# Kernel tuning notes

Measured on AMD Instinct MI355X. Metric: run time of the kernel, lower is better.

The kernel has to match this reference:

```python
import jax, jax.numpy as jnp
import numpy as np

N_NODES = 50000
N_EDGES = 800000
IN_C, HID_C, OUT_C = 128, 128, 64


def setup_inputs() -> dict:
    key = jax.random.key(0)
    k = jax.random.split(key, 8)
    x = jax.random.normal(k[0], (N_NODES, IN_C), dtype=jnp.float32)
    edge_index = jax.random.randint(k[1], (2, N_EDGES), 0, N_NODES, dtype=jnp.int64)
    edge_weight = jax.random.uniform(k[2], (N_EDGES,), dtype=jnp.float32)
    # GCNConv parameters (glorot-style scale)
    W1 = jax.random.normal(k[3], (IN_C, HID_C), dtype=jnp.float32) * (1.0 / np.sqrt(IN_C))
    b1 = jnp.zeros((HID_C,), dtype=jnp.float32)
    W2 = jax.random.normal(k[4], (HID_C, OUT_C), dtype=jnp.float32) * (1.0 / np.sqrt(HID_C))
    b2 = jnp.zeros((OUT_C,), dtype=jnp.float32)
    return {"x": x, "edge_index": edge_index, "edge_weight": edge_weight,
            "W1": W1, "b1": b1, "W2": W2, "b2": b2}


def _gcn_conv(x, src, dst, edge_weight, W, b, num_nodes):
    # GCNConv(normalize=False): out[i] = sum_{(j->i) in E} w_ji * (x[j] @ W) + b
    h = x @ W                                  # [N, C_out] dense GEMM first (cheaper than per-edge)
    msg = h[src]                               # [E, C_out] gather
    if edge_weight is not None:
        msg = msg * edge_weight[:, None]
    agg = jax.ops.segment_sum(msg, dst, num_segments=num_nodes)  # scatter-add
    return agg + b


def reference(x, edge_index, edge_weight, W1, b1, W2, b2):
    # Eval mode: F.dropout(training=False) is identity.
    src, dst = edge_index[0], edge_index[1]
    n = x.shape[0]
    h = _gcn_conv(x, src, dst, edge_weight, W1, b1, n)
    h = jax.nn.relu(h)
    out = _gcn_conv(h, src, dst, None, W2, b2, n)  # second conv: no edge_weight
    return out
```

## Files before the change

kernel.cpp:

```cpp
#include <hip/hip_runtime.h>
#include <hip/hip_fp8.h>

#define N_NODES 50000
#define N_EDGES 800000
#define IN_C    128
#define HID_C   128
#define OUT_C   64

#define EPB     4096
#define SC_BLOCKS 196
#define NBUCKET 196
#define CAP     6144
#define G1_BLOCKS 782

typedef unsigned int       uint32;
typedef unsigned short     ushort16;
typedef unsigned char      uchar8;
typedef unsigned long long u64;
typedef __attribute__((ext_vector_type(8))) short short8;
typedef __attribute__((ext_vector_type(4))) float f32x4;

__device__ __forceinline__ ushort16 f2bf(float f) {
    uint32 u = __float_as_uint(f);
    u += 0x7FFFu + ((u >> 16) & 1u);
    return (ushort16)(u >> 16);
}
__device__ __forceinline__ ushort16 f2h_bits(float f) {
    union { _Float16 h; ushort16 u; } cv;
    cv.h = (_Float16)f;
    return cv.u;
}
__device__ __forceinline__ float h_bits2f(uint32 bits) {
    union { ushort16 u; _Float16 h; } cv;
    cv.u = (ushort16)bits;
    return (float)cv.h;
}
__device__ __forceinline__ uchar8 f2fp8(float f) {
    __hip_fp8_e4m3 t(f);
    return *reinterpret_cast<unsigned char*>(&t);
}
__device__ __forceinline__ float fp82f(uchar8 b) {
    __hip_fp8_e4m3 t;
    *reinterpret_cast<unsigned char*>(&t) = b;
    return (float)t;
}
__device__ __forceinline__ void fp8x4_wacc(uint32 v, float w, f32x4& a) {
    a.x += w * fp82f((uchar8)(v & 0xFF));
    a.y += w * fp82f((uchar8)((v >> 8) & 0xFF));
    a.z += w * fp82f((uchar8)((v >> 16) & 0xFF));
    a.w += w * fp82f((uchar8)(v >> 24));
}
__device__ __forceinline__ void fp8x4_acc(uint32 v, f32x4& a) {
    a.x += fp82f((uchar8)(v & 0xFF));
    a.y += fp82f((uchar8)((v >> 8) & 0xFF));
    a.z += fp82f((uchar8)((v >> 16) & 0xFF));
    a.w += fp82f((uchar8)(v >> 24));
}
__device__ __forceinline__ void bfly4(f32x4& a, int d) {
    a.x += __shfl_xor(a.x, d); a.y += __shfl_xor(a.y, d);
    a.z += __shfl_xor(a.z, d); a.w += __shfl_xor(a.w, d);
}
__device__ __forceinline__ uint32 packbf(float a, float b) {
    return (uint32)f2bf(a) | ((uint32)f2bf(b) << 16);
}

__global__ __launch_bounds__(256) void prep_w_kernel(const float* __restrict__ W1,
                                                     const float* __restrict__ W2,
                                                     ushort16* __restrict__ W1t,
                                                     ushort16* __restrict__ W2t,
                                                     int* __restrict__ cursorC) {
    if (blockIdx.x == 0 && threadIdx.x < NBUCKET) cursorC[threadIdx.x] = 0;
    int i = blockIdx.x * 256 + threadIdx.x;
    if (i < 128 * 128) {
        int n = i / 128, k = i % 128;
        W1t[i] = f2bf(W1[k * 128 + n]);
    }
    int j = i - 128 * 128;
    if (j >= 0 && j < 64 * 128) {
        int n = j / 128, k = j % 128;
        W2t[j] = f2bf(W2[k * 64 + n]);
    }
}

__global__ __launch_bounds__(256) void gemm1_scatter_kernel(const float* __restrict__ x,
                                                            const ushort16* __restrict__ W1t,
                                                            uchar8* __restrict__ H1,
                                                            const int* __restrict__ ei,
                                                            const float* __restrict__ ew,
                                                            int* __restrict__ cursorC,
                                                            u64* __restrict__ ebuf) {
    __shared__ char smem[52224];
    const int tid = threadIdx.x;

    if (blockIdx.x < SC_BLOCKS) {
        int* hist  = (int*)smem;
        int* lbase = (int*)(smem + 1024);
        int blk = blockIdx.x;
        hist[tid] = 0;
        __syncthreads();
        int base = blk * EPB;
        int    bv[EPB / 256];
        uint32 pkv[EPB / 256];
        ushort16 wv[EPB / 256];
#pragma unroll
        for (int k = 0; k < EPB / 256; k++) {
            int e = base + tid + k * 256;
            if (e < N_EDGES) {
                int dst = ei[N_EDGES + e];
                int src = ei[e];
                float w = ew[e];
                bv[k]  = dst >> 8;
                pkv[k] = ((uint32)(dst & 255) << 16) | (uint32)src;
                wv[k]  = f2h_bits(w);
                atomicAdd(&hist[bv[k]], 1);
            } else bv[k] = -1;
        }
        __syncthreads();
        int n = hist[tid];
        lbase[tid] = n ? atomicAdd(&cursorC[tid], n) : 0;
        __syncthreads();
        hist[tid] = 0;
        __syncthreads();
#pragma unroll
        for (int k = 0; k < EPB / 256; k++) {
            if (bv[k] >= 0) {
                int b = bv[k];
                int r = atomicAdd(&hist[b], 1);
                int pos = lbase[b] + r;
                if (pos < CAP)
                    ebuf[(size_t)b * CAP + pos] = ((u64)wv[k] << 32) | pkv[k];
            }
        }
        return;
    }

    typedef ushort16 row136[136];
    row136* As = (row136*)smem;
    row136* Ws = (row136*)(smem + 64 * 136 * 2);

    const int wave = tid >> 6;
    const int lane = tid & 63;
    const int quad = lane >> 4;
    const int m    = lane & 15;
    const int blockRow = (blockIdx.x - SC_BLOCKS) * 64;

#pragma unroll
    for (int p = 0; p < 8; p++) {
        int u = tid + 256 * p;
        int row = u / 16, c8 = u % 16;
        uint4 v = ((const uint4*)W1t)[u];
        *((uint4*)&Ws[row][c8 * 8]) = v;
    }
#pragma unroll
    for (int p = 0; p < 8; p++) {
        int u = tid + 256 * p;
        int row = u / 32, c4 = u % 32;
        int gr = blockRow + row; if (gr > N_NODES - 1) gr = N_NODES - 1;
        float4 v = ((const float4*)x)[gr * 32 + c4];
        ushort4 s;
        s.x = f2bf(v.x); s.y = f2bf(v.y); s.z = f2bf(v.z); s.w = f2bf(v.w);
        *((ushort4*)&As[row][c4 * 4]) = s;
    }
    __syncthreads();

    f32x4 acc[8];
#pragma unroll
    for (int nt = 0; nt < 8; nt++) acc[nt] = (f32x4){0.f, 0.f, 0.f, 0.f};

#pragma unroll
    for (int kc = 0; kc < 128; kc += 32) {
        short8 a = *((const short8*)&As[wave * 16 + m][kc + quad * 8]);
#pragma unroll
        for (int nt = 0; nt < 8; nt++) {
            short8 b = *((const short8*)&Ws[nt * 16 + m][kc + quad * 8]);
            acc[nt] = __builtin_amdgcn_mfma_f32_16x16x32_bf16(a, b, acc[nt], 0, 0, 0);
        }
    }

    __syncthreads();
    uchar8* c8lds = (uchar8*)&As[0][0];
#pragma unroll
    for (int nt = 0; nt < 8; nt++)
#pragma unroll
        for (int r = 0; r < 4; r++)
            c8lds[(wave * 16 + quad * 4 + r) * 128 + nt * 16 + m] = f2fp8(acc[nt][r]);
    __syncthreads();
#pragma unroll
    for (int p = 0; p < 2; p++) {
        int u = tid + 256 * p;
        int row = u / 8, c16 = u % 8;
        int gr = blockRow + row;
        if (gr < N_NODES)
            ((uint4*)H1)[gr * 8 + c16] = *((const uint4*)&c8lds[row * 128 + c16 * 16]);
    }
}

__global__ __launch_bounds__(1024) void csr_fine_kernel(const u64* __restrict__ ebuf,
                                                        const int* __restrict__ cursorC,
                                                        int* __restrict__ rowStart,
                                                        int* __restrict__ rowEnd,
                                                        uint32* __restrict__ pairs) {
    __shared__ uint32   keys[CAP];
    __shared__ ushort16 ws[CAP];
    __shared__ int hist[256];
    __shared__ int scan[256];
    int b = blockIdx.x, t = threadIdx.x;
    int s = b * CAP;
    int len = cursorC[b];
    if (len > CAP) len = CAP;
    if (t < 256) hist[t] = 0;
    __syncthreads();
    for (int j = t; j < len; j += 1024) {
        u64 kv = ebuf[s + j];
        uint32 lo = (uint32)kv;
        keys[j] = lo;
        ws[j]   = (ushort16)(kv >> 32);
        atomicAdd(&hist[lo >> 16], 1);
    }
    __syncthreads();
    if (t < 256) scan[t] = hist[t];
    __syncthreads();
    for (int off = 1; off < 256; off <<= 1) {
        int a = 0;
        if (t < 256 && t >= off) a = scan[t - off];
        __syncthreads();
        if (t < 256) scan[t] += a;
        __syncthreads();
    }
    if (t < 256) {
        int excl = scan[t] - hist[t];
        hist[t] = excl;
        int node = b * 256 + t;
        if (node < N_NODES) {
            rowStart[node] = s + excl;
            rowEnd[node]   = s + scan[t];
        }
    }
    __syncthreads();
    for (int j = t; j < len; j += 1024) {
        uint32 kv = keys[j];
        int r = atomicAdd(&hist[kv >> 16], 1);
        pairs[s + r] = (kv & 0xFFFFu) | ((uint32)ws[j] << 16);
    }
}

template<int NT, bool ABF16, bool OUTFP8>
__global__ __launch_bounds__(256) void mfma_gemm_kernel(const void* __restrict__ Aptr,
                                                        const ushort16* __restrict__ Wt,
                                                        void* __restrict__ Cout, int M) {
    constexpr int N = NT * 16;
    __shared__ ushort16 As[64][136];
    __shared__ ushort16 Ws[N][136];

    const int tid  = threadIdx.x;
    const int wave = tid >> 6;
    const int lane = tid & 63;
    const int quad = lane >> 4;
    const int m    = lane & 15;
    const int blockRow = blockIdx.x * 64;

#pragma unroll
    for (int p = 0; p < N * 16 / 256; p++) {
        int u = tid + 256 * p;
        int row = u / 16, c8 = u % 16;
        uint4 v = ((const uint4*)Wt)[u];
        *((uint4*)&Ws[row][c8 * 8]) = v;
    }
    if (ABF16) {
#pragma unroll
        for (int p = 0; p < 4; p++) {
            int u = tid + 256 * p;
            int row = u / 16, c8 = u % 16;
            int gr = blockRow + row; if (gr > M - 1) gr = M - 1;
            uint4 v = ((const uint4*)Aptr)[gr * 16 + c8];
            *((uint4*)&As[row][c8 * 8]) = v;
        }
    } else {
#pragma unroll
        for (int p = 0; p < 8; p++) {
            int u = tid + 256 * p;
            int row = u / 32, c4 = u % 32;
            int gr = blockRow + row; if (gr > M - 1) gr = M - 1;
            float4 v = ((const float4*)Aptr)[gr * 32 + c4];
            ushort4 s;
            s.x = f2bf(v.x); s.y = f2bf(v.y); s.z = f2bf(v.z); s.w = f2bf(v.w);
            *((ushort4*)&As[row][c4 * 4]) = s;
        }
    }
    __syncthreads();

    f32x4 acc[NT];
#pragma unroll
    for (int nt = 0; nt < NT; nt++) acc[nt] = (f32x4){0.f, 0.f, 0.f, 0.f};

#pragma unroll
    for (int kc = 0; kc < 128; kc += 32) {
        short8 a = *((const short8*)&As[wave * 16 + m][kc + quad * 8]);
#pragma unroll
        for (int nt = 0; nt < NT; nt++) {
            short8 b = *((const short8*)&Ws[nt * 16 + m][kc + quad * 8]);
            acc[nt] = __builtin_amdgcn_mfma_f32_16x16x32_bf16(a, b, acc[nt], 0, 0, 0);
        }
    }

    __syncthreads();
    if (OUTFP8) {
        uchar8* c8lds = (uchar8*)&As[0][0];
#pragma unroll
        for (int nt = 0; nt < NT; nt++)
#pragma unroll
            for (int r = 0; r < 4; r++)
                c8lds[(wave * 16 + quad * 4 + r) * N + nt * 16 + m] = f2fp8(acc[nt][r]);
        __syncthreads();
#pragma unroll
        for (int p = 0; p < 64 * N / 16 / 256; p++) {
            int u = tid + 256 * p;
            int row = u / (N / 16), c16 = u % (N / 16);
            int gr = blockRow + row;
            if (gr < M)
                ((uint4*)Cout)[gr * (N / 16) + c16] = *((const uint4*)&c8lds[row * N + c16 * 16]);
        }
    } else {
#pragma unroll
        for (int nt = 0; nt < NT; nt++)
#pragma unroll
            for (int r = 0; r < 4; r++)
                As[wave * 16 + quad * 4 + r][nt * 16 + m] = f2bf(acc[nt][r]);
        __syncthreads();
#pragma unroll
        for (int p = 0; p < 64 * N / 8 / 256; p++) {
            int u = tid + 256 * p;
            int row = u / (N / 8), c8 = u % (N / 8);
            int gr = blockRow + row;
            if (gr < M)
                ((uint4*)Cout)[gr * (N / 8) + c8] = *((const uint4*)&As[row][c8 * 8]);
        }
    }
}

__global__ __launch_bounds__(256) void agg1_kernel(const uint4* __restrict__ H1,
                                                   const int* __restrict__ rowStart,
                                                   const int* __restrict__ rowEnd,
                                                   const uint32* __restrict__ pairs,
                                                   const float* __restrict__ b1,
                                                   uint4* __restrict__ A1) {
    int node = blockIdx.x * 4 + (threadIdx.x >> 6);
    int lane = threadIdx.x & 63;
    int oct = lane >> 3, cl = lane & 7;
    if (node >= N_NODES) return;
    int s = rowStart[node], e = rowEnd[node];
    f32x4 aA = (f32x4){0.f,0.f,0.f,0.f}, aB = aA, aC = aA, aD = aA;
    int i = s + oct;
    for (; i + 8 < e; i += 16) {
        uint32 p0 = pairs[i], p1 = pairs[i + 8];
        uint4 h0 = H1[(p0 & 0xFFFFu) * 8 + cl];
        uint4 h1 = H1[(p1 & 0xFFFFu) * 8 + cl];
        float w0 = h_bits2f(p0 >> 16), w1 = h_bits2f(p1 >> 16);
        fp8x4_wacc(h0.x, w0, aA); fp8x4_wacc(h0.y, w0, aB);
        fp8x4_wacc(h0.z, w0, aC); fp8x4_wacc(h0.w, w0, aD);
        fp8x4_wacc(h1.x, w1, aA); fp8x4_wacc(h1.y, w1, aB);
        fp8x4_wacc(h1.z, w1, aC); fp8x4_wacc(h1.w, w1, aD);
    }
    for (; i < e; i += 8) {
        uint32 p = pairs[i];
        uint4 h = H1[(p & 0xFFFFu) * 8 + cl];
        float w = h_bits2f(p >> 16);
        fp8x4_wacc(h.x, w, aA); fp8x4_wacc(h.y, w, aB);
        fp8x4_wacc(h.z, w, aC); fp8x4_wacc(h.w, w, aD);
    }
#pragma unroll
    for (int d = 8; d <= 32; d <<= 1) {
        bfly4(aA, d); bfly4(aB, d); bfly4(aC, d); bfly4(aD, d);
    }
    if (oct == 0) {
        const float4* b1f = (const float4*)b1;
        float4 b0 = b1f[cl * 4], b4 = b1f[cl * 4 + 1], b8 = b1f[cl * 4 + 2], bc = b1f[cl * 4 + 3];
        uint4 r0, r1;
        r0.x = packbf(fmaxf(aA.x + b0.x, 0.f), fmaxf(aA.y + b0.y, 0.f));
        r0.y = packbf(fmaxf(aA.z + b0.z, 0.f), fmaxf(aA.w + b0.w, 0.f));
        r0.z = packbf(fmaxf(aB.x + b4.x, 0.f), fmaxf(aB.y + b4.y, 0.f));
        r0.w = packbf(fmaxf(aB.z + b4.z, 0.f), fmaxf(aB.w + b4.w, 0.f));
        r1.x = packbf(fmaxf(aC.x + b8.x, 0.f), fmaxf(aC.y + b8.y, 0.f));
        r1.y = packbf(fmaxf(aC.z + b8.z, 0.f), fmaxf(aC.w + b8.w, 0.f));
        r1.z = packbf(fmaxf(aD.x + bc.x, 0.f), fmaxf(aD.y + bc.y, 0.f));
        r1.w = packbf(fmaxf(aD.z + bc.z, 0.f), fmaxf(aD.w + bc.w, 0.f));
        A1[node * 16 + cl * 2]     = r0;
        A1[node * 16 + cl * 2 + 1] = r1;
    }
}

__global__ __launch_bounds__(256) void agg2_kernel(const uint2* __restrict__ H2,
                                                   const int* __restrict__ rowStart,
                                                   const int* __restrict__ rowEnd,
                                                   const uint32* __restrict__ pairs,
                                                   const float* __restrict__ b2,
                                                   float4* __restrict__ out) {
    int node = blockIdx.x * 4 + (threadIdx.x >> 6);
    int lane = threadIdx.x & 63;
    int oct = lane >> 3, cl = lane & 7;
    if (node >= N_NODES) return;
    int s = rowStart[node], e = rowEnd[node];
    f32x4 aX = (f32x4){0.f,0.f,0.f,0.f}, aY = aX;
    int i = s + oct;
    for (; i + 8 < e; i += 16) {
        uint32 p0 = pairs[i], p1 = pairs[i + 8];
        uint2 v0 = H2[(p0 & 0xFFFFu) * 8 + cl];
        uint2 v1 = H2[(p1 & 0xFFFFu) * 8 + cl];
        fp8x4_acc(v0.x, aX); fp8x4_acc(v0.y, aY);
        fp8x4_acc(v1.x, aX); fp8x4_acc(v1.y, aY);
    }
    for (; i < e; i += 8) {
        uint2 v = H2[(pairs[i] & 0xFFFFu) * 8 + cl];
        fp8x4_acc(v.x, aX); fp8x4_acc(v.y, aY);
    }
#pragma unroll
    for (int d = 8; d <= 32; d <<= 1) { bfly4(aX, d); bfly4(aY, d); }
    if (oct == 0) {
        const float4* b2f = (const float4*)b2;
        float4 bx = b2f[cl * 2], by = b2f[cl * 2 + 1];
        float4 rx, ry;
        rx.x = aX.x + bx.x; rx.y = aX.y + bx.y; rx.z = aX.z + bx.z; rx.w = aX.w + bx.w;
        ry.x = aY.x + by.x; ry.y = aY.y + by.y; ry.z = aY.z + by.z; ry.w = aY.w + by.w;
        out[node * 16 + cl * 2]     = rx;
        out[node * 16 + cl * 2 + 1] = ry;
    }
}

extern "C" void kernel_launch(void* const* d_in, const int* in_sizes, int n_in,
                              void* d_out, int out_size, void* d_ws, size_t ws_size,
                              hipStream_t stream) {
    const float* x  = (const float*)d_in[0];
    const int*   ei = (const int*)  d_in[1];
    const float* ew = (const float*)d_in[2];
    const float* W1 = (const float*)d_in[3];
    const float* b1 = (const float*)d_in[4];
    const float* W2 = (const float*)d_in[5];
    const float* b2 = (const float*)d_in[6];
    float* out = (float*)d_out;

    uint32* H1      = (uint32*)d_ws;
    uint32* A1      = H1 + (size_t)N_NODES * 32;
    uint32* H2      = A1 + (size_t)N_NODES * 64;
    uint32* pairs   = H2 + (size_t)N_NODES * 16;
    u64* ebuf       = (u64*)(pairs + (size_t)NBUCKET * CAP);
    ushort16* W1t   = (ushort16*)(ebuf + (size_t)NBUCKET * CAP);
    ushort16* W2t   = W1t + 128 * 128;
    int* cursorC    = (int*)(W2t + 64 * 128);
    int* rowStart   = cursorC + ((NBUCKET + 1) & ~1);
    int* rowEnd     = rowStart + N_NODES;

    const int nodeBlocks = (N_NODES + 3) / 4;

    prep_w_kernel<<<96, 256, 0, stream>>>(W1, W2, W1t, W2t, cursorC);

    gemm1_scatter_kernel<<<SC_BLOCKS + G1_BLOCKS, 256, 0, stream>>>(
        x, W1t, (uchar8*)H1, ei, ew, cursorC, ebuf);

    csr_fine_kernel<<<NBUCKET, 1024, 0, stream>>>(ebuf, cursorC, rowStart, rowEnd, pairs);

    agg1_kernel<<<nodeBlocks, 256, 0, stream>>>((const uint4*)H1, rowStart, rowEnd, pairs, b1, (uint4*)A1);

    mfma_gemm_kernel<4, true, true><<<G1_BLOCKS, 256, 0, stream>>>(A1, W2t, H2, N_NODES);

    agg2_kernel<<<nodeBlocks, 256, 0, stream>>>((const uint2*)H2, rowStart, rowEnd, pairs, b2, (float4*)out);
}
```

Measured before the change: 164.2 us.

## Drop weight-prep kernel, convert weights inline, and double scatter block count

```diff
diff --git a/kernel.cpp b/kernel.cpp
--- a/kernel.cpp
+++ b/kernel.cpp
@@ -7,8 +7,8 @@
 #define HID_C   128
 #define OUT_C   64
 
-#define EPB     4096
-#define SC_BLOCKS 196
+#define EPB     2048
+#define SC_BLOCKS 391
 #define NBUCKET 196
 #define CAP     6144
 #define G1_BLOCKS 782
@@ -64,26 +64,8 @@
     return (uint32)f2bf(a) | ((uint32)f2bf(b) << 16);
 }
 
-__global__ __launch_bounds__(256) void prep_w_kernel(const float* __restrict__ W1,
-                                                     const float* __restrict__ W2,
-                                                     ushort16* __restrict__ W1t,
-                                                     ushort16* __restrict__ W2t,
-                                                     int* __restrict__ cursorC) {
-    if (blockIdx.x == 0 && threadIdx.x < NBUCKET) cursorC[threadIdx.x] = 0;
-    int i = blockIdx.x * 256 + threadIdx.x;
-    if (i < 128 * 128) {
-        int n = i / 128, k = i % 128;
-        W1t[i] = f2bf(W1[k * 128 + n]);
-    }
-    int j = i - 128 * 128;
-    if (j >= 0 && j < 64 * 128) {
-        int n = j / 128, k = j % 128;
-        W2t[j] = f2bf(W2[k * 64 + n]);
-    }
-}
-
 __global__ __launch_bounds__(256) void gemm1_scatter_kernel(const float* __restrict__ x,
-                                                            const ushort16* __restrict__ W1t,
+                                                            const float* __restrict__ W1,
                                                             uchar8* __restrict__ H1,
                                                             const int* __restrict__ ei,
                                                             const float* __restrict__ ew,
@@ -147,9 +129,11 @@
 #pragma unroll
     for (int p = 0; p < 8; p++) {
         int u = tid + 256 * p;
-        int row = u / 16, c8 = u % 16;
-        uint4 v = ((const uint4*)W1t)[u];
-        *((uint4*)&Ws[row][c8 * 8]) = v;
+        int n = u & 127, k0 = (u >> 7) * 8;
+        ushort16 tmp[8];
+#pragma unroll
+        for (int j = 0; j < 8; j++) tmp[j] = f2bf(W1[(k0 + j) * 128 + n]);
+        *((uint4*)&Ws[n][k0]) = *((const uint4*)tmp);
     }
 #pragma unroll
     for (int p = 0; p < 8; p++) {
@@ -244,13 +228,11 @@
     }
 }
 
-template<int NT, bool ABF16, bool OUTFP8>
-__global__ __launch_bounds__(256) void mfma_gemm_kernel(const void* __restrict__ Aptr,
-                                                        const ushort16* __restrict__ Wt,
-                                                        void* __restrict__ Cout, int M) {
-    constexpr int N = NT * 16;
+__global__ __launch_bounds__(256) void gemm2_kernel(const uint32* __restrict__ A1,
+                                                    const float* __restrict__ W2,
+                                                    uchar8* __restrict__ H2) {
     __shared__ ushort16 As[64][136];
-    __shared__ ushort16 Ws[N][136];
+    __shared__ ushort16 Ws[64][136];
 
     const int tid  = threadIdx.x;
     const int wave = tid >> 6;
@@ -260,81 +242,52 @@
     const int blockRow = blockIdx.x * 64;
 
 #pragma unroll
-    for (int p = 0; p < N * 16 / 256; p++) {
+    for (int p = 0; p < 4; p++) {
+        int u = tid + 256 * p;
+        int n = u & 63, k0 = (u >> 6) * 8;
+        ushort16 tmp[8];
+#pragma unroll
+        for (int j = 0; j < 8; j++) tmp[j] = f2bf(W2[(k0 + j) * 64 + n]);
+        *((uint4*)&Ws[n][k0]) = *((const uint4*)tmp);
+    }
+#pragma unroll
+    for (int p = 0; p < 4; p++) {
         int u = tid + 256 * p;
         int row = u / 16, c8 = u % 16;
-        uint4 v = ((const uint4*)Wt)[u];
-        *((uint4*)&Ws[row][c8 * 8]) = v;
-    }
-    if (ABF16) {
-#pragma unroll
-        for (int p = 0; p < 4; p++) {
-            int u = tid + 256 * p;
-            int row = u / 16, c8 = u % 16;
-            int gr = blockRow + row; if (gr > M - 1) gr = M - 1;
-            uint4 v = ((const uint4*)Aptr)[gr * 16 + c8];
-            *((uint4*)&As[row][c8 * 8]) = v;
-        }
-    } else {
-#pragma unroll
-        for (int p = 0; p < 8; p++) {
-            int u = tid + 256 * p;
-            int row = u / 32, c4 = u % 32;
-            int gr = blockRow + row; if (gr > M - 1) gr = M - 1;
-            float4 v = ((const float4*)Aptr)[gr * 32 + c4];
-            ushort4 s;
-            s.x = f2bf(v.x); s.y = f2bf(v.y); s.z = f2bf(v.z); s.w = f2bf(v.w);
-            *((ushort4*)&As[row][c4 * 4]) = s;
-        }
-    }
-    __syncthreads();
-
-    f32x4 acc[NT];
-#pragma unroll
-    for (int nt = 0; nt < NT; nt++) acc[nt] = (f32x4){0.f, 0.f, 0.f, 0.f};
+        int gr = blockRow + row; if (gr > N_NODES - 1) gr = N_NODES - 1;
+        uint4 v = ((const uint4*)A1)[gr * 16 + c8];
+        *((uint4*)&As[row][c8 * 8]) = v;
+    }
+    __syncthreads();
+
+    f32x4 acc[4];
+#pragma unroll
+    for (int nt = 0; nt < 4; nt++) acc[nt] = (f32x4){0.f, 0.f, 0.f, 0.f};
 
 #pragma unroll
     for (int kc = 0; kc < 128; kc += 32) {
         short8 a = *((const short8*)&As[wave * 16 + m][kc + quad * 8]);
 #pragma unroll
-        for (int nt = 0; nt < NT; nt++) {
+        for (int nt = 0; nt < 4; nt++) {
             short8 b = *((const short8*)&Ws[nt * 16 + m][kc + quad * 8]);
             acc[nt] = __builtin_amdgcn_mfma_f32_16x16x32_bf16(a, b, acc[nt], 0, 0, 0);
         }
     }
 
     __syncthreads();
-    if (OUTFP8) {
-        uchar8* c8lds = (uchar8*)&As[0][0];
-#pragma unroll
-        for (int nt = 0; nt < NT; nt++)
-#pragma unroll
-            for (int r = 0; r < 4; r++)
-                c8lds[(wave * 16 + quad * 4 + r) * N + nt * 16 + m] = f2fp8(acc[nt][r]);
-        __syncthreads();
-#pragma unroll
-        for (int p = 0; p < 64 * N / 16 / 256; p++) {
-            int u = tid + 256 * p;
-            int row = u / (N / 16), c16 = u % (N / 16);
-            int gr = blockRow + row;
-            if (gr < M)
-                ((uint4*)Cout)[gr * (N / 16) + c16] = *((const uint4*)&c8lds[row * N + c16 * 16]);
-        }
-    } else {
-#pragma unroll
-        for (int nt = 0; nt < NT; nt++)
-#pragma unroll
-            for (int r = 0; r < 4; r++)
-                As[wave * 16 + quad * 4 + r][nt * 16 + m] = f2bf(acc[nt][r]);
-        __syncthreads();
-#pragma unroll
-        for (int p = 0; p < 64 * N / 8 / 256; p++) {
-            int u = tid + 256 * p;
-            int row = u / (N / 8), c8 = u % (N / 8);
-            int gr = blockRow + row;
-            if (gr < M)
-                ((uint4*)Cout)[gr * (N / 8) + c8] = *((const uint4*)&As[row][c8 * 8]);
-        }
+    uchar8* c8lds = (uchar8*)&As[0][0];
+#pragma unroll
+    for (int nt = 0; nt < 4; nt++)
+#pragma unroll
+        for (int r = 0; r < 4; r++)
+            c8lds[(wave * 16 + quad * 4 + r) * 64 + nt * 16 + m] = f2fp8(acc[nt][r]);
+    __syncthreads();
+    {
+        int u = tid;
+        int row = u / 4, c16 = u % 4;
+        int gr = blockRow + row;
+        if (gr < N_NODES)
+            ((uint4*)H2)[gr * 4 + c16] = *((const uint4*)&c8lds[row * 64 + c16 * 16]);
     }
 }
 
@@ -443,24 +396,22 @@
     uint32* H2      = A1 + (size_t)N_NODES * 64;
     uint32* pairs   = H2 + (size_t)N_NODES * 16;
     u64* ebuf       = (u64*)(pairs + (size_t)NBUCKET * CAP);
-    ushort16* W1t   = (ushort16*)(ebuf + (size_t)NBUCKET * CAP);
-    ushort16* W2t   = W1t + 128 * 128;
-    int* cursorC    = (int*)(W2t + 64 * 128);
+    int* cursorC    = (int*)(ebuf + (size_t)NBUCKET * CAP);
     int* rowStart   = cursorC + ((NBUCKET + 1) & ~1);
     int* rowEnd     = rowStart + N_NODES;
 
     const int nodeBlocks = (N_NODES + 3) / 4;
 
-    prep_w_kernel<<<96, 256, 0, stream>>>(W1, W2, W1t, W2t, cursorC);
+    hipMemsetAsync(cursorC, 0, NBUCKET * sizeof(int), stream);
 
     gemm1_scatter_kernel<<<SC_BLOCKS + G1_BLOCKS, 256, 0, stream>>>(
-        x, W1t, (uchar8*)H1, ei, ew, cursorC, ebuf);
+        x, W1, (uchar8*)H1, ei, ew, cursorC, ebuf);
 
     csr_fine_kernel<<<NBUCKET, 1024, 0, stream>>>(ebuf, cursorC, rowStart, rowEnd, pairs);
 
     agg1_kernel<<<nodeBlocks, 256, 0, stream>>>((const uint4*)H1, rowStart, rowEnd, pairs, b1, (uint4*)A1);
 
-    mfma_gemm_kernel<4, true, true><<<G1_BLOCKS, 256, 0, stream>>>(A1, W2t, H2, N_NODES);
+    gemm2_kernel<<<G1_BLOCKS, 256, 0, stream>>>(A1, W2, (uchar8*)H2);
 
     agg2_kernel<<<nodeBlocks, 256, 0, stream>>>((const uint2*)H2, rowStart, rowEnd, pairs, b2, (float4*)out);
 }
```

Result: slower. 168.4 us (+2.6%).
